# Kernel tuning notes

Measured on AMD Instinct MI355X. Metric: run time of the kernel, lower is better.

## Reference

```python
import jax, jax.numpy as jnp
import numpy as np

B, L, D, C, H, M = 256, 500, 3, 32, 512, 5
I = D + C            # per-step input dim (dihedrals concat condition)
O = D * M            # out_dim * num_mixtures


def setup_inputs() -> dict:
    key = jax.random.key(0)
    ks = jax.random.split(key, 6)
    return {
        "inputs": jax.random.normal(ks[0], (B, L, D), dtype=jnp.float32),
        "z": jax.random.normal(ks[1], (B, L, C), dtype=jnp.float32),
        "W_enc": jax.random.normal(ks[2], (L, I, H), dtype=jnp.float32),
        "b_enc": jnp.zeros((1, H), dtype=jnp.float32),
        "V_mu": jax.random.normal(ks[3], (L, H, O), dtype=jnp.float32),
        "b_mu": jnp.zeros((L, 1, O), dtype=jnp.float32),
        "V_sigma": jax.random.normal(ks[4], (L, H, O), dtype=jnp.float32),
        "b_sigma": jnp.zeros((L, 1, O), dtype=jnp.float32),
        "V_pi": jax.random.normal(ks[5], (L, H, M), dtype=jnp.float32),
        "b_pi": jnp.zeros((L, 1, M), dtype=jnp.float32),
    }


def reference(inputs, z, W_enc, b_enc, V_mu, b_mu, V_sigma, b_sigma, V_pi, b_pi):
    # x: [L, B, I]
    x = jnp.transpose(jnp.concatenate([inputs, z], axis=2), (1, 0, 2))
    # per-step contributions c[i] = x[i] @ W_enc[i] -> [L, B, H]
    c = jnp.einsum('lbi,lih->lbh', x, W_enc)
    # a[i] = b_enc + sum_{j<i} c[j]  (exclusive prefix sum of the recurrence)
    csum = jnp.cumsum(c, axis=0)
    a = jnp.concatenate([jnp.zeros_like(csum[:1]), csum[:-1]], axis=0) + b_enc
    h = jax.nn.relu(a)  # [L, B, H]
    h_mu = jnp.einsum('lbh,lho->lbo', h, V_mu) + b_mu        # [L, B, O]
    h_sigma = jnp.einsum('lbh,lho->lbo', h, V_sigma) + b_sigma
    h_pi = jnp.einsum('lbh,lhm->lbm', h, V_pi) + b_pi        # [L, B, M]
    logits = jnp.concatenate([h_mu, h_sigma, h_pi], axis=2)  # [L, B, 2O+M]
    return jnp.transpose(logits, (1, 0, 2))                  # [B, L, 2O+M]
```

## Files before the change

kernel.cpp:

```cpp
#include <hip/hip_runtime.h>

constexpr int B = 256, L = 500, D = 3, C = 32, I = 35, H = 512, O = 15, M = 5;
constexpr int KP1 = 48;
constexpr int JP = 48;
constexpr int KPV = 520;
constexpr int G = 100;
constexpr int LC = 5;

typedef __attribute__((ext_vector_type(8))) _Float16 half8;
typedef __attribute__((ext_vector_type(2))) _Float16 half2;
typedef __attribute__((ext_vector_type(16))) float f32x16;

__global__ __launch_bounds__(256, 2) void kPrep(const float* __restrict__ inp,
                                                const float* __restrict__ z,
                                                const float* __restrict__ W,
                                                const float* __restrict__ Vmu,
                                                const float* __restrict__ Vsg,
                                                const float* __restrict__ Vpi,
                                                _Float16* __restrict__ xT,
                                                _Float16* __restrict__ Wt,
                                                _Float16* __restrict__ Vt) {
  const int bx = blockIdx.x, tid = threadIdx.x;

  if (bx < L) {
    const int l = bx, b = tid;
    float e[36];
    const float* ip = inp + ((size_t)b * L + l) * D;
    e[0] = ip[0]; e[1] = ip[1]; e[2] = ip[2];
    const float4* zp = (const float4*)(z + ((size_t)b * L + l) * C);
#pragma unroll
    for (int q = 0; q < 8; ++q) {
      float4 v = zp[q];
      e[D + 4 * q + 0] = v.x; e[D + 4 * q + 1] = v.y;
      e[D + 4 * q + 2] = v.z; e[D + 4 * q + 3] = v.w;
    }
    e[35] = 0.f;
    unsigned u[24];
#pragma unroll
    for (int q = 0; q < 18; ++q)
      u[q] = __builtin_bit_cast(unsigned, __builtin_amdgcn_cvt_pkrtz(e[2 * q], e[2 * q + 1]));
#pragma unroll
    for (int q = 18; q < 24; ++q) u[q] = 0u;
    uint4* dst = (uint4*)(xT + ((size_t)l * B + b) * KP1);
#pragma unroll
    for (int q = 0; q < 6; ++q) dst[q] = ((const uint4*)u)[q];
  } else if (bx < 3 * L) {
    const int t = bx - L;
    const int l = t >> 1, hp = t & 1;
    const int h = tid + 256 * hp;
    float v[36];
#pragma unroll
    for (int i = 0; i < I; ++i) v[i] = W[((size_t)l * I + i) * H + h];
    v[35] = 0.f;
    unsigned u[24];
#pragma unroll
    for (int q = 0; q < 18; ++q)
      u[q] = __builtin_bit_cast(unsigned, __builtin_amdgcn_cvt_pkrtz(v[2 * q], v[2 * q + 1]));
#pragma unroll
    for (int q = 18; q < 24; ++q) u[q] = 0u;
    uint4* dst = (uint4*)(Wt + ((size_t)l * H + h) * KP1);
#pragma unroll
    for (int q = 0; q < 6; ++q) dst[q] = ((const uint4*)u)[q];
  } else {
    const int l = bx - 3 * L;
    const int w = tid >> 6, lane = tid & 63;
    const int h0 = lane * 8;
    for (int row = w; row < 35; row += 4) {
      const float* src;
      int j, od;
      if (row < O)          { src = Vmu + (size_t)l * H * O; j = row;         od = O; }
      else if (row < 2 * O) { src = Vsg + (size_t)l * H * O; j = row - O;     od = O; }
      else                  { src = Vpi + (size_t)l * H * M; j = row - 2 * O; od = M; }
      float v[8];
#pragma unroll
      for (int e = 0; e < 8; ++e) v[e] = src[(size_t)(h0 + e) * od + j];
      unsigned u[4];
#pragma unroll
      for (int q = 0; q < 4; ++q)
        u[q] = __builtin_bit_cast(unsigned, __builtin_amdgcn_cvt_pkrtz(v[2 * q], v[2 * q + 1]));
      *(uint4*)(Vt + ((size_t)l * JP + row) * KPV + h0) = (uint4){u[0], u[1], u[2], u[3]};
    }
  }
}

__global__ __launch_bounds__(256, 3) void kA(const _Float16* __restrict__ xT,
                                             const _Float16* __restrict__ Wt,
                                             _Float16* __restrict__ S) {
  const int idx = blockIdx.x;
  const int g = ((idx >> 6) << 3) + (idx & 7);
  if (g >= G) return;
  const int b0 = ((idx >> 3) & 7) * 32;
  const int w = threadIdx.x >> 6, lane = threadIdx.x & 63;
  const int ln31 = lane & 31, hi32 = lane >> 5;

  f32x16 acc[4];
#pragma unroll
  for (int mt = 0; mt < 4; ++mt)
#pragma unroll
    for (int r = 0; r < 16; ++r) acc[mt][r] = 0.f;

#pragma unroll
  for (int t = 0; t < LC; ++t) {
    const int l = g * LC + t;
    const _Float16* Xb = xT + ((size_t)l * B + b0 + ln31) * KP1 + 8 * hi32;
    const _Float16* Wb = Wt + ((size_t)l * H + 128 * w + ln31) * KP1 + 8 * hi32;
    half8 xf[3], wf[12];
#pragma unroll
    for (int kt = 0; kt < 3; ++kt) xf[kt] = *(const half8*)(Xb + 16 * kt);
#pragma unroll
    for (int mt = 0; mt < 4; ++mt)
#pragma unroll
      for (int kt = 0; kt < 3; ++kt)
        wf[mt * 3 + kt] = *(const half8*)(Wb + (size_t)mt * 32 * KP1 + 16 * kt);
#pragma unroll
    for (int mt = 0; mt < 4; ++mt)
#pragma unroll
      for (int kt = 0; kt < 3; ++kt)
        acc[mt] = __builtin_amdgcn_mfma_f32_32x32x16_f16(wf[mt * 3 + kt], xf[kt], acc[mt], 0, 0, 0);
  }
  _Float16* Sp = S + ((size_t)g * H + 128 * w) * B + b0 + ln31;
#pragma unroll
  for (int mt = 0; mt < 4; ++mt)
#pragma unroll
    for (int r = 0; r < 16; ++r) {
      const int hl = 32 * mt + (r & 3) + 8 * (r >> 2) + 4 * hi32;
      Sp[(size_t)hl * B] = (_Float16)acc[mt][r];
    }
}

__global__ __launch_bounds__(256) void kS(const _Float16* __restrict__ S,
                                          const float* __restrict__ benc,
                                          _Float16* __restrict__ Acc) {
  const int t = blockIdx.x * 256 + threadIdx.x;
  const int b = t & (B - 1), h = t >> 8;
  float run = benc[h];
  const _Float16* sp = S + (size_t)h * B + b;
  _Float16* ap = Acc + (size_t)h * B + b;
  constexpr size_t stride = (size_t)H * B;
#pragma unroll 5
  for (int g = 0; g < G; ++g) {
    ap[g * stride] = (_Float16)run;
    run += (float)sp[g * stride];
  }
}

__global__ __launch_bounds__(256, 2) void kB(const _Float16* __restrict__ xT,
                                             const _Float16* __restrict__ Wt,
                                             const _Float16* __restrict__ Vt,
                                             const _Float16* __restrict__ Acc,
                                             const float* __restrict__ bmu,
                                             const float* __restrict__ bsg,
                                             const float* __restrict__ bpi,
                                             float* __restrict__ out) {
  const int idx = blockIdx.x;
  const int g = ((idx >> 6) << 3) + (idx & 7);
  if (g >= G) return;
  const int b0 = ((idx >> 3) & 7) * 32;
  const int tid = threadIdx.x;
  const int w = tid >> 6, lane = tid & 63;
  const int ln31 = lane & 31, hi32 = lane >> 5;

  __shared__ _Float16 po[4][LC][32][36];
  __shared__ float bias_s[LC][35];

  if (tid < LC * 35) {
    const int t = tid / 35, j = tid - 35 * t, l = g * LC + t;
    bias_s[t][j] = (j < O) ? bmu[l * O + j]
                 : (j < 2 * O) ? bsg[l * O + (j - O)]
                 : bpi[l * M + (j - 2 * O)];
  }

  f32x16 acc[4];
  const _Float16* Ap = Acc + ((size_t)g * H + 128 * w) * B + b0 + ln31;
#pragma unroll
  for (int mt = 0; mt < 4; ++mt)
#pragma unroll
    for (int r = 0; r < 16; ++r) {
      const int hl = 32 * mt + (r & 3) + 8 * (r >> 2) + 4 * hi32;
      acc[mt][r] = (float)Ap[(size_t)hl * B];
    }

#pragma unroll 1
  for (int t = 0; t < LC; ++t) {
    const int l = g * LC + t;
    const _Float16* Vb = Vt + (size_t)l * JP * KPV + 128 * w + 8 * hi32;
    half8 va0[8];
#pragma unroll
    for (int s = 0; s < 8; ++s)
      va0[s] = *(const half8*)(Vb + 16 * s + (size_t)ln31 * KPV);
    half8 va1[8];
#pragma unroll
    for (int s = 0; s < 8; ++s) {
      va1[s] = half8{};
      if (ln31 < 3)
        va1[s] = *(const half8*)(Vb + 16 * s + (size_t)(32 + ln31) * KPV);
    }
    half8 xf[3], wf[12];
    if (t != LC - 1) {
      const _Float16* Xb = xT + ((size_t)l * B + b0 + ln31) * KP1 + 8 * hi32;
      const _Float16* Wb = Wt + ((size_t)l * H + 128 * w + ln31) * KP1 + 8 * hi32;
#pragma unroll
      for (int kt = 0; kt < 3; ++kt) xf[kt] = *(const half8*)(Xb + 16 * kt);
#pragma unroll
      for (int mt = 0; mt < 4; ++mt)
#pragma unroll
        for (int kt = 0; kt < 3; ++kt)
          wf[mt * 3 + kt] = *(const half8*)(Wb + (size_t)mt * 32 * KP1 + 16 * kt);
    }
    f32x16 o0, o1;
#pragma unroll
    for (int r = 0; r < 16; ++r) { o0[r] = 0.f; o1[r] = 0.f; }
#pragma unroll
    for (int mt = 0; mt < 4; ++mt) {
      unsigned P0[4], P1[4];
#pragma unroll
      for (int m = 0; m < 4; ++m) {
        float e0 = fmaxf(acc[mt][4 * m + 0], 0.f);
        float e1 = fmaxf(acc[mt][4 * m + 1], 0.f);
        float e2 = fmaxf(acc[mt][4 * m + 2], 0.f);
        float e3 = fmaxf(acc[mt][4 * m + 3], 0.f);
        P0[m] = __builtin_bit_cast(unsigned, __builtin_amdgcn_cvt_pkrtz(e0, e1));
        P1[m] = __builtin_bit_cast(unsigned, __builtin_amdgcn_cvt_pkrtz(e2, e3));
      }
#pragma unroll
      for (int tl = 0; tl < 2; ++tl) {
        unsigned w0 = P0[2 * tl], w2 = P0[2 * tl + 1];
        unsigned w1 = P1[2 * tl], w3 = P1[2 * tl + 1];
        asm("v_permlane32_swap_b32 %0, %1" : "+v"(w0), "+v"(w2));
        asm("v_permlane32_swap_b32 %0, %1" : "+v"(w1), "+v"(w3));
        half2 a0 = __builtin_bit_cast(half2, w0);
        half2 a1 = __builtin_bit_cast(half2, w1);
        half2 a2 = __builtin_bit_cast(half2, w2);
        half2 a3 = __builtin_bit_cast(half2, w3);
        half8 hb = {a0.x, a0.y, a1.x, a1.y, a2.x, a2.y, a3.x, a3.y};
        o0 = __builtin_amdgcn_mfma_f32_32x32x16_f16(va0[2 * mt + tl], hb, o0, 0, 0, 0);
        o1 = __builtin_amdgcn_mfma_f32_32x32x16_f16(va1[2 * mt + tl], hb, o1, 0, 0, 0);
      }
    }
    _Float16* pw = &po[w][t][ln31][0];
#pragma unroll
    for (int r = 0; r < 16; r += 2) {
      const int j0 = (r & 3) + 8 * (r >> 2) + 4 * hi32;
      *(unsigned*)&pw[j0] =
          __builtin_bit_cast(unsigned, __builtin_amdgcn_cvt_pkrtz(o0[r], o0[r + 1]));
    }
    if (hi32 == 0) {
      *(unsigned*)&pw[32] =
          __builtin_bit_cast(unsigned, __builtin_amdgcn_cvt_pkrtz(o1[0], o1[1]));
      pw[34] = (_Float16)o1[2];
    }
    if (t != LC - 1) {
#pragma unroll
      for (int mt = 0; mt < 4; ++mt)
#pragma unroll
        for (int kt = 0; kt < 3; ++kt)
          acc[mt] = __builtin_amdgcn_mfma_f32_32x32x16_f16(wf[mt * 3 + kt], xf[kt], acc[mt], 0, 0, 0);
    }
  }
  __syncthreads();
  for (int f = tid; f < 32 * LC * 35; f += 256) {
    const int b = f / (LC * 35);
    const int r = f - b * (LC * 35);
    const int t = r / 35, j = r - 35 * t;
    const float s = (float)po[0][t][b][j] + (float)po[1][t][b][j] +
                    (float)po[2][t][b][j] + (float)po[3][t][b][j];
    out[((size_t)(b0 + b) * L + g * LC + t) * 35 + j] = s + bias_s[t][j];
  }
}

extern "C" void kernel_launch(void* const* d_in, const int* in_sizes, int n_in,
                              void* d_out, int out_size, void* d_ws, size_t ws_size,
                              hipStream_t stream) {
  const float* inp  = (const float*)d_in[0];
  const float* z    = (const float*)d_in[1];
  const float* Wenc = (const float*)d_in[2];
  const float* benc = (const float*)d_in[3];
  const float* Vmu  = (const float*)d_in[4];
  const float* bmu  = (const float*)d_in[5];
  const float* Vsg  = (const float*)d_in[6];
  const float* bsg  = (const float*)d_in[7];
  const float* Vpi  = (const float*)d_in[8];
  const float* bpi  = (const float*)d_in[9];
  float* out = (float*)d_out;

  char* ws = (char*)d_ws;
  _Float16* xT  = (_Float16*)ws;
  _Float16* Wt  = (_Float16*)(ws + 12288000);
  _Float16* Vt  = (_Float16*)(ws + 36864000);
  _Float16* S   = (_Float16*)(ws + 61824000);
  _Float16* Acc = (_Float16*)(ws + 88038400);

  kPrep<<<dim3(4 * L), 256, 0, stream>>>(inp, z, Wenc, Vmu, Vsg, Vpi, xT, Wt, Vt);
  kA<<<dim3(832), 256, 0, stream>>>(xT, Wt, S);
  kS<<<dim3(B * H / 256), 256, 0, stream>>>(S, benc, Acc);
  kB<<<dim3(832), 256, 0, stream>>>(xT, Wt, Vt, Acc, bmu, bsg, bpi, out);
}
```

Measured before the change: 236.0 us.

## Fuse x and W_enc fp32-to-fp16 conversion into GEMM kernels, drop prep buffers

```diff
diff --git a/kernel.cpp b/kernel.cpp
--- a/kernel.cpp
+++ b/kernel.cpp
@@ -1,7 +1,6 @@
 #include <hip/hip_runtime.h>
 
 constexpr int B = 256, L = 500, D = 3, C = 32, I = 35, H = 512, O = 15, M = 5;
-constexpr int KP1 = 48;
 constexpr int JP = 48;
 constexpr int KPV = 520;
 constexpr int G = 100;
@@ -11,80 +10,76 @@
 typedef __attribute__((ext_vector_type(2))) _Float16 half2;
 typedef __attribute__((ext_vector_type(16))) float f32x16;
 
-__global__ __launch_bounds__(256, 2) void kPrep(const float* __restrict__ inp,
-                                                const float* __restrict__ z,
-                                                const float* __restrict__ W,
-                                                const float* __restrict__ Vmu,
-                                                const float* __restrict__ Vsg,
-                                                const float* __restrict__ Vpi,
-                                                _Float16* __restrict__ xT,
-                                                _Float16* __restrict__ Wt,
-                                                _Float16* __restrict__ Vt) {
-  const int bx = blockIdx.x, tid = threadIdx.x;
-
-  if (bx < L) {
-    const int l = bx, b = tid;
-    float e[36];
-    const float* ip = inp + ((size_t)b * L + l) * D;
-    e[0] = ip[0]; e[1] = ip[1]; e[2] = ip[2];
-    const float4* zp = (const float4*)(z + ((size_t)b * L + l) * C);
-#pragma unroll
-    for (int q = 0; q < 8; ++q) {
-      float4 v = zp[q];
-      e[D + 4 * q + 0] = v.x; e[D + 4 * q + 1] = v.y;
-      e[D + 4 * q + 2] = v.z; e[D + 4 * q + 3] = v.w;
-    }
-    e[35] = 0.f;
-    unsigned u[24];
-#pragma unroll
-    for (int q = 0; q < 18; ++q)
-      u[q] = __builtin_bit_cast(unsigned, __builtin_amdgcn_cvt_pkrtz(e[2 * q], e[2 * q + 1]));
-#pragma unroll
-    for (int q = 18; q < 24; ++q) u[q] = 0u;
-    uint4* dst = (uint4*)(xT + ((size_t)l * B + b) * KP1);
-#pragma unroll
-    for (int q = 0; q < 6; ++q) dst[q] = ((const uint4*)u)[q];
-  } else if (bx < 3 * L) {
-    const int t = bx - L;
-    const int l = t >> 1, hp = t & 1;
-    const int h = tid + 256 * hp;
-    float v[36];
-#pragma unroll
-    for (int i = 0; i < I; ++i) v[i] = W[((size_t)l * I + i) * H + h];
-    v[35] = 0.f;
-    unsigned u[24];
-#pragma unroll
-    for (int q = 0; q < 18; ++q)
+__device__ __forceinline__ half8 pk8(float a0, float a1, float a2, float a3,
+                                     float a4, float a5, float a6, float a7) {
+  half2 p0 = __builtin_bit_cast(half2, __builtin_amdgcn_cvt_pkrtz(a0, a1));
+  half2 p1 = __builtin_bit_cast(half2, __builtin_amdgcn_cvt_pkrtz(a2, a3));
+  half2 p2 = __builtin_bit_cast(half2, __builtin_amdgcn_cvt_pkrtz(a4, a5));
+  half2 p3 = __builtin_bit_cast(half2, __builtin_amdgcn_cvt_pkrtz(a6, a7));
+  return (half8){p0.x, p0.y, p1.x, p1.y, p2.x, p2.y, p3.x, p3.y};
+}
+
+__device__ __forceinline__ void load_x(const float* __restrict__ inp,
+                                       const float* __restrict__ z,
+                                       int l, int b, int hi32, half8 xf[3]) {
+  const float* zr = z + ((size_t)b * L + l) * C + 8 * hi32;
+  float4 z0 = *(const float4*)zr, z1 = *(const float4*)(zr + 4);
+  float4 z2 = *(const float4*)(zr + 16), z3 = *(const float4*)(zr + 20);
+  xf[0] = pk8(z0.x, z0.y, z0.z, z0.w, z1.x, z1.y, z1.z, z1.w);
+  xf[1] = pk8(z2.x, z2.y, z2.z, z2.w, z3.x, z3.y, z3.z, z3.w);
+  const float* ip = inp + ((size_t)b * L + l) * D;
+  float i0 = ip[0], i1 = ip[1], i2 = ip[2];
+  if (hi32) { i0 = 0.f; i1 = 0.f; i2 = 0.f; }
+  xf[2] = pk8(i0, i1, i2, 0.f, 0.f, 0.f, 0.f, 0.f);
+}
+
+__device__ __forceinline__ void load_w(const float* __restrict__ W,
+                                       int l, int hbase, int ln31, int hi32,
+                                       half8 wf[12]) {
+  const float* Wc = W + (size_t)l * I * H + hbase + ln31;
+#pragma unroll
+  for (int mt = 0; mt < 4; ++mt) {
+    const float* Wm = Wc + 32 * mt;
+    float a[8], bq[8];
+#pragma unroll
+    for (int e = 0; e < 8; ++e) a[e] = Wm[(size_t)(3 + 8 * hi32 + e) * H];
+#pragma unroll
+    for (int e = 0; e < 8; ++e) bq[e] = Wm[(size_t)(19 + 8 * hi32 + e) * H];
+    wf[mt * 3 + 0] = pk8(a[0], a[1], a[2], a[3], a[4], a[5], a[6], a[7]);
+    wf[mt * 3 + 1] = pk8(bq[0], bq[1], bq[2], bq[3], bq[4], bq[5], bq[6], bq[7]);
+    float c0 = Wm[0], c1 = Wm[(size_t)H], c2 = Wm[(size_t)2 * H];
+    if (hi32) { c0 = 0.f; c1 = 0.f; c2 = 0.f; }
+    wf[mt * 3 + 2] = pk8(c0, c1, c2, 0.f, 0.f, 0.f, 0.f, 0.f);
+  }
+}
+
+__global__ __launch_bounds__(256) void kV(const float* __restrict__ Vmu,
+                                          const float* __restrict__ Vsg,
+                                          const float* __restrict__ Vpi,
+                                          _Float16* __restrict__ Vt) {
+  const int l = blockIdx.x, tid = threadIdx.x;
+  const int w = tid >> 6, lane = tid & 63;
+  const int h0 = lane * 8;
+  for (int row = w; row < 35; row += 4) {
+    const float* src;
+    int j, od;
+    if (row < O)          { src = Vmu + (size_t)l * H * O; j = row;         od = O; }
+    else if (row < 2 * O) { src = Vsg + (size_t)l * H * O; j = row - O;     od = O; }
+    else                  { src = Vpi + (size_t)l * H * M; j = row - 2 * O; od = M; }
+    float v[8];
+#pragma unroll
+    for (int e = 0; e < 8; ++e) v[e] = src[(size_t)(h0 + e) * od + j];
+    unsigned u[4];
+#pragma unroll
+    for (int q = 0; q < 4; ++q)
       u[q] = __builtin_bit_cast(unsigned, __builtin_amdgcn_cvt_pkrtz(v[2 * q], v[2 * q + 1]));
-#pragma unroll
-    for (int q = 18; q < 24; ++q) u[q] = 0u;
-    uint4* dst = (uint4*)(Wt + ((size_t)l * H + h) * KP1);
-#pragma unroll
-    for (int q = 0; q < 6; ++q) dst[q] = ((const uint4*)u)[q];
-  } else {
-    const int l = bx - 3 * L;
-    const int w = tid >> 6, lane = tid & 63;
-    const int h0 = lane * 8;
-    for (int row = w; row < 35; row += 4) {
-      const float* src;
-      int j, od;
-      if (row < O)          { src = Vmu + (size_t)l * H * O; j = row;         od = O; }
-      else if (row < 2 * O) { src = Vsg + (size_t)l * H * O; j = row - O;     od = O; }
-      else                  { src = Vpi + (size_t)l * H * M; j = row - 2 * O; od = M; }
-      float v[8];
-#pragma unroll
-      for (int e = 0; e < 8; ++e) v[e] = src[(size_t)(h0 + e) * od + j];
-      unsigned u[4];
-#pragma unroll
-      for (int q = 0; q < 4; ++q)
-        u[q] = __builtin_bit_cast(unsigned, __builtin_amdgcn_cvt_pkrtz(v[2 * q], v[2 * q + 1]));
-      *(uint4*)(Vt + ((size_t)l * JP + row) * KPV + h0) = (uint4){u[0], u[1], u[2], u[3]};
-    }
-  }
-}
-
-__global__ __launch_bounds__(256, 3) void kA(const _Float16* __restrict__ xT,
-                                             const _Float16* __restrict__ Wt,
+    *(uint4*)(Vt + ((size_t)l * JP + row) * KPV + h0) = (uint4){u[0], u[1], u[2], u[3]};
+  }
+}
+
+__global__ __launch_bounds__(256, 2) void kA(const float* __restrict__ inp,
+                                             const float* __restrict__ z,
+                                             const float* __restrict__ W,
                                              _Float16* __restrict__ S) {
   const int idx = blockIdx.x;
   const int g = ((idx >> 6) << 3) + (idx & 7);
@@ -102,16 +97,9 @@
 #pragma unroll
   for (int t = 0; t < LC; ++t) {
     const int l = g * LC + t;
-    const _Float16* Xb = xT + ((size_t)l * B + b0 + ln31) * KP1 + 8 * hi32;
-    const _Float16* Wb = Wt + ((size_t)l * H + 128 * w + ln31) * KP1 + 8 * hi32;
     half8 xf[3], wf[12];
-#pragma unroll
-    for (int kt = 0; kt < 3; ++kt) xf[kt] = *(const half8*)(Xb + 16 * kt);
-#pragma unroll
-    for (int mt = 0; mt < 4; ++mt)
-#pragma unroll
-      for (int kt = 0; kt < 3; ++kt)
-        wf[mt * 3 + kt] = *(const half8*)(Wb + (size_t)mt * 32 * KP1 + 16 * kt);
+    load_x(inp, z, l, b0 + ln31, hi32, xf);
+    load_w(W, l, 128 * w, ln31, hi32, wf);
 #pragma unroll
     for (int mt = 0; mt < 4; ++mt)
 #pragma unroll
@@ -144,8 +132,9 @@
   }
 }
 
-__global__ __launch_bounds__(256, 2) void kB(const _Float16* __restrict__ xT,
-                                             const _Float16* __restrict__ Wt,
+__global__ __launch_bounds__(256, 2) void kB(const float* __restrict__ inp,
+                                             const float* __restrict__ z,
+                                             const float* __restrict__ W,
                                              const _Float16* __restrict__ Vt,
                                              const _Float16* __restrict__ Acc,
                                              const float* __restrict__ bmu,
@@ -197,15 +186,8 @@
     }
     half8 xf[3], wf[12];
     if (t != LC - 1) {
-      const _Float16* Xb = xT + ((size_t)l * B + b0 + ln31) * KP1 + 8 * hi32;
-      const _Float16* Wb = Wt + ((size_t)l * H + 128 * w + ln31) * KP1 + 8 * hi32;
-#pragma unroll
-      for (int kt = 0; kt < 3; ++kt) xf[kt] = *(const half8*)(Xb + 16 * kt);
-#pragma unroll
-      for (int mt = 0; mt < 4; ++mt)
-#pragma unroll
-        for (int kt = 0; kt < 3; ++kt)
-          wf[mt * 3 + kt] = *(const half8*)(Wb + (size_t)mt * 32 * KP1 + 16 * kt);
+      load_x(inp, z, l, b0 + ln31, hi32, xf);
+      load_w(W, l, 128 * w, ln31, hi32, wf);
     }
     f32x16 o0, o1;
 #pragma unroll
@@ -284,14 +266,12 @@
   float* out = (float*)d_out;
 
   char* ws = (char*)d_ws;
-  _Float16* xT  = (_Float16*)ws;
-  _Float16* Wt  = (_Float16*)(ws + 12288000);
-  _Float16* Vt  = (_Float16*)(ws + 36864000);
-  _Float16* S   = (_Float16*)(ws + 61824000);
-  _Float16* Acc = (_Float16*)(ws + 88038400);
-
-  kPrep<<<dim3(4 * L), 256, 0, stream>>>(inp, z, Wenc, Vmu, Vsg, Vpi, xT, Wt, Vt);
-  kA<<<dim3(832), 256, 0, stream>>>(xT, Wt, S);
+  _Float16* Vt  = (_Float16*)ws;
+  _Float16* S   = (_Float16*)(ws + 24960000);
+  _Float16* Acc = (_Float16*)(ws + 51174400);
+
+  kV<<<dim3(L), 256, 0, stream>>>(Vmu, Vsg, Vpi, Vt);
+  kA<<<dim3(832), 256, 0, stream>>>(inp, z, Wenc, S);
   kS<<<dim3(B * H / 256), 256, 0, stream>>>(S, benc, Acc);
-  kB<<<dim3(832), 256, 0, stream>>>(xT, Wt, Vt, Acc, bmu, bsg, bpi, out);
-}
+  kB<<<dim3(832), 256, 0, stream>>>(inp, z, Wenc, Vt, Acc, bmu, bsg, bpi, out);
+}
```

Result: slower. 269.7 us (+14.2%).
